# Kernel optimization log

Measured on AMD Instinct MI355X. Metric: run time of the kernel, lower is better.

## Reference

```python
import jax, jax.numpy as jnp
import numpy as np

H = 128  # LSTM units per direction


def _lstm_last_state(x_proj, Wr, b):
    """x_proj: [T,B,4H] precomputed input projection. Returns final hidden [B,H]."""
    B = x_proj.shape[1]
    h0 = jnp.zeros((B, H), x_proj.dtype)
    c0 = jnp.zeros((B, H), x_proj.dtype)

    def step(carry, xt):
        h, c = carry
        z = xt + h @ Wr + b  # [B,4H]
        i, f, g, o = jnp.split(z, 4, axis=-1)  # keras gate order: i, f, c(g), o
        i = jax.nn.sigmoid(i)
        f = jax.nn.sigmoid(f)
        g = jnp.tanh(g)
        o = jax.nn.sigmoid(o)
        c = f * c + i * g
        h = o * jnp.tanh(c)
        return (h, c), None

    (h, c), _ = jax.lax.scan(step, (h0, c0), x_proj)
    return h


def setup_inputs() -> dict:
    key = jax.random.key(0)
    ks = jax.random.split(key, 8)
    B, T, D = 128, 256, 1024
    s_in = 1.0 / np.sqrt(D)
    s_rec = 1.0 / np.sqrt(H)
    return {
        "x": jax.random.normal(ks[0], (B, T, D), jnp.float32),  # precomputed ELMo embeddings
        "Wf_k": jax.random.normal(ks[1], (D, 4 * H), jnp.float32) * s_in,
        "Wf_r": jax.random.normal(ks[2], (H, 4 * H), jnp.float32) * s_rec,
        "bf": jnp.zeros((4 * H,), jnp.float32),
        "Wb_k": jax.random.normal(ks[3], (D, 4 * H), jnp.float32) * s_in,
        "Wb_r": jax.random.normal(ks[4], (H, 4 * H), jnp.float32) * s_rec,
        "bb": jnp.zeros((4 * H,), jnp.float32),
        "W1": jax.random.normal(ks[5], (2 * H, 32), jnp.float32) * (1.0 / np.sqrt(2 * H)),
        "b1": jnp.zeros((32,), jnp.float32),
        "W2": jax.random.normal(ks[6], (32, 2), jnp.float32) * (1.0 / np.sqrt(32)),
        "b2": jnp.zeros((2,), jnp.float32),
    }


def reference(x, Wf_k, Wf_r, bf, Wb_k, Wb_r, bb, W1, b1, W2, b2):
    # Bidirectional LSTM over ELMo embeddings x: [B,T,D]; dropout inactive (inference).
    xp_f = jnp.einsum('btd,dg->tbg', x, Wf_k)            # [T,B,4H]
    h_fwd = _lstm_last_state(xp_f, Wf_r, bf)             # [B,H]
    xp_b = jnp.einsum('btd,dg->tbg', x[:, ::-1, :], Wb_k)
    h_bwd = _lstm_last_state(xp_b, Wb_r, bb)             # [B,H]
    h = jnp.concatenate([h_fwd, h_bwd], axis=-1)         # [B,2H]
    y = jax.nn.relu(h @ W1 + b1)                          # [B,32]
    return jax.nn.sigmoid(y @ W2 + b2)                    # [B,2]
```

## Files before the change

### kernel.cpp

```cpp
#include <hip/hip_runtime.h>
#include <cstdint>
#include <cstddef>


typedef __attribute__((ext_vector_type(8))) short short8;
typedef __attribute__((ext_vector_type(4))) float f32x4;
typedef __attribute__((address_space(1))) unsigned int gas_uint;
typedef __attribute__((address_space(3))) unsigned int las_uint;
typedef __attribute__((address_space(1))) const unsigned short as1_us;

__device__ __forceinline__ unsigned short f2b(float f) {
    unsigned int u = __float_as_uint(f);
    u += 0x7FFFu + ((u >> 16) & 1u);
    return (unsigned short)(u >> 16);
}
__device__ __forceinline__ float b2f(unsigned short u) {
    return __uint_as_float(((unsigned int)u) << 16);
}
__device__ __forceinline__ float rcp_(float x) { return __builtin_amdgcn_rcpf(x); }
__device__ __forceinline__ float sigmoidf_(float z) { return rcp_(1.0f + __expf(-z)); }
__device__ __forceinline__ float tanhf_(float z) {
    float e = __expf(2.0f * z);
    return 1.0f - 2.0f * rcp_(e + 1.0f);
}

#define LITE_BARRIER() asm volatile("s_waitcnt lgkmcnt(0)\n\ts_barrier" ::: "memory")

__device__ __forceinline__ void async_ld16(const unsigned short* g, unsigned short* l) {
    __builtin_amdgcn_global_load_lds(
        (gas_uint*)(uintptr_t)g,
        (las_uint*)(uintptr_t)(unsigned int)(uintptr_t)l,
        16, 0, 0);
}

__global__ void conv_x(const float* __restrict__ x, unsigned short* __restrict__ xb, int n8) {
    int idx = blockIdx.x * blockDim.x + threadIdx.x;
    int stride = gridDim.x * blockDim.x;
    for (int i = idx; i < n8; i += stride) {
        const float4* p = ((const float4*)x) + (size_t)i * 2;
        float4 a = p[0], b = p[1];
        short8 r;
        r[0] = (short)f2b(a.x); r[1] = (short)f2b(a.y);
        r[2] = (short)f2b(a.z); r[3] = (short)f2b(a.w);
        r[4] = (short)f2b(b.x); r[5] = (short)f2b(b.y);
        r[6] = (short)f2b(b.z); r[7] = (short)f2b(b.w);
        *(((short8*)xb) + i) = r;
    }
}

__global__ void conv_wk(const float* __restrict__ wf, const float* __restrict__ wb,
                        unsigned short* __restrict__ wt) {
    int dir = blockIdx.y;
    const float* w = dir ? wb : wf;
    int id = blockIdx.x * blockDim.x + threadIdx.x;
    int g = id >> 10, d = id & 1023;
    wt[(size_t)dir * 524288 + id] = f2b(w[d * 512 + g]);
}

__global__ __launch_bounds__(256, 2) void gemm_xp(
    const unsigned short* __restrict__ A,
    const unsigned short* __restrict__ Wt,
    const float* __restrict__ bf_, const float* __restrict__ bb_,
    unsigned short* __restrict__ XP)
{
    __shared__ unsigned short As[128 * 64];
    __shared__ unsigned short Bs[128 * 64];

    const int tid  = threadIdx.x;

    const int flat = blockIdx.x + 256 * (blockIdx.y + 4 * blockIdx.z);
    const int xcd  = flat & 7;
    const int p    = flat >> 3;
    const int tn   = p & 3;
    const int dir  = (p >> 2) & 1;
    const int tm   = xcd * 32 + (p >> 3);

    const int w    = tid >> 6;
    const int lane = tid & 63;
    const int lanelo = lane & 15;
    const int quad = lane >> 4;
    const int wm = w & 1, wn = w >> 1;

    const unsigned short* Bmat = Wt + (size_t)dir * 524288;
    const float* bias = dir ? bb_ : bf_;
    unsigned short* out = XP + (size_t)dir * 16777216;

    const unsigned short* ga[4];
    const unsigned short* gb[4];
    unsigned short* la[4];
    unsigned short* lb[4];
#pragma unroll
    for (int c = 0; c < 4; ++c) {
        int p2 = c * 256 + tid;
        int row = p2 >> 3;
        int lc = (p2 & 7) ^ (row & 7);
        ga[c] = A    + (size_t)(tm * 128 + row) * 1024 + lc * 8;
        gb[c] = Bmat + (size_t)(tn * 128 + row) * 1024 + lc * 8;
        int ub = (c * 256 + (tid & ~63)) * 8;
        la[c] = As + ub;
        lb[c] = Bs + ub;
    }

    f32x4 acc[4][4];
#pragma unroll
    for (int i = 0; i < 4; i++)
#pragma unroll
        for (int j = 0; j < 4; j++) acc[i][j] = (f32x4){0.f, 0.f, 0.f, 0.f};

    for (int kt = 0; kt < 16; ++kt) {
        __syncthreads();
#pragma unroll
        for (int c = 0; c < 4; ++c) {
            async_ld16(ga[c] + kt * 64, la[c]);
            async_ld16(gb[c] + kt * 64, lb[c]);
        }
        __syncthreads();
#pragma unroll
        for (int ks = 0; ks < 2; ++ks) {
            short8 af[4], bfr[4];
#pragma unroll
            for (int i = 0; i < 4; ++i) {
                int row = wm * 64 + i * 16 + lanelo;
                af[i] = *(const short8*)(As + row * 64 + (((ks * 4 + quad) ^ (row & 7)) * 8));
            }
#pragma unroll
            for (int j = 0; j < 4; ++j) {
                int row = wn * 64 + j * 16 + lanelo;
                bfr[j] = *(const short8*)(Bs + row * 64 + (((ks * 4 + quad) ^ (row & 7)) * 8));
            }
#pragma unroll
            for (int i = 0; i < 4; ++i)
#pragma unroll
                for (int j = 0; j < 4; ++j)
                    acc[i][j] = __builtin_amdgcn_mfma_f32_16x16x32_bf16(af[i], bfr[j], acc[i][j], 0, 0, 0);
        }
    }

    float biasv[4];
#pragma unroll
    for (int j = 0; j < 4; ++j)
        biasv[j] = bias[tn * 128 + wn * 64 + j * 16 + lanelo];

#pragma unroll
    for (int i = 0; i < 4; ++i) {
#pragma unroll
        for (int r = 0; r < 4; ++r) {
            int gr = tm * 128 + wm * 64 + i * 16 + quad * 4 + r;
            int bb = gr >> 8, tt = gr & 255;
            size_t orow = (size_t)(tt * 128 + bb) * 512;
#pragma unroll
            for (int j = 0; j < 4; ++j) {
                int col = tn * 128 + wn * 64 + j * 16 + lanelo;
                out[orow + col] = f2b(acc[i][j][r] + biasv[j]);
            }
        }
    }
}

__global__ __launch_bounds__(512, 2) void lstm_rec(
    const unsigned short* __restrict__ XP,
    const float* __restrict__ Wfr, const float* __restrict__ Wbr,
    float* __restrict__ Hout)
{
    __shared__ unsigned short h_lds[2][128];

    const int tid    = threadIdx.x;
    const int w      = tid >> 6;
    const int lane   = tid & 63;
    const int lanelo = lane & 15;
    const int quad   = lane >> 4;
    const int dir    = blockIdx.x >> 7;
    const int seq    = blockIdx.x & 127;
    const int dim    = w * 16 + lanelo;

    const float* Wr = dir ? Wbr : Wfr;
    const unsigned short* xp = XP + (size_t)dir * 16777216;

    short8 wrf[4][4];
#pragma unroll
    for (int g = 0; g < 4; ++g)
#pragma unroll
        for (int ks = 0; ks < 4; ++ks) {
            short8 f;
#pragma unroll
            for (int j = 0; j < 8; ++j)
                f[j] = (short)f2b(Wr[(size_t)(ks * 32 + quad * 8 + j) * 512 + g * 128 + dim]);
            wrf[g][ks] = f;
        }

    if (tid < 128) ((unsigned short*)h_lds)[tid] = 0;

    float cv = 0.f, hv = 0.f;

    const ptrdiff_t xstep = dir ? -65536 : 65536;
    const unsigned short* xb_ =
        xp + (size_t)(dir ? 255 : 0) * 65536 + (size_t)seq * 512 + dim;

    unsigned int xA[4], xB[4], xC[4], xD[4];

#define XLOAD(BUF)                                                               \
    {                                                                            \
        const as1_us* xg = (const as1_us*)(uintptr_t)xb_;                        \
        _Pragma("unroll")                                                        \
        for (int g = 0; g < 4; ++g) BUF[g] = xg[g * 128];                        \
        xb_ += xstep;                                                            \
    }

    XLOAD(xA)
    XLOAD(xB)
    XLOAD(xC)
    XLOAD(xD)

    LITE_BARRIER();

    const f32x4 kZ = (f32x4){0.f, 0.f, 0.f, 0.f};

#define LSTM_STEP(XC_, CUR, NXT)                                                 \
    {                                                                            \
               \
        float xv0 = b2f((unsigned short)XC_[0]);                                 \
        float xv1 = b2f((unsigned short)XC_[1]);                                 \
        float xv2 = b2f((unsigned short)XC_[2]);                                 \
        float xv3 = b2f((unsigned short)XC_[3]);                                 \
        XLOAD(XC_)                                                               \
         \
        short8 hfrag[4];                                                         \
        _Pragma("unroll")                                                        \
        for (int ks = 0; ks < 4; ++ks)                                           \
            hfrag[ks] = *(const short8*)(&h_lds[CUR][ks * 32 + quad * 8]);       \
            \
        f32x4 z0 = __builtin_amdgcn_mfma_f32_16x16x32_bf16(hfrag[0], wrf[0][0], kZ, 0, 0, 0); \
        f32x4 z1 = __builtin_amdgcn_mfma_f32_16x16x32_bf16(hfrag[0], wrf[1][0], kZ, 0, 0, 0); \
        f32x4 z2 = __builtin_amdgcn_mfma_f32_16x16x32_bf16(hfrag[0], wrf[2][0], kZ, 0, 0, 0); \
        f32x4 z3 = __builtin_amdgcn_mfma_f32_16x16x32_bf16(hfrag[0], wrf[3][0], kZ, 0, 0, 0); \
        _Pragma("unroll")                                                        \
        for (int ks = 1; ks < 4; ++ks) {                                         \
            z0 = __builtin_amdgcn_mfma_f32_16x16x32_bf16(hfrag[ks], wrf[0][ks], z0, 0, 0, 0); \
            z1 = __builtin_amdgcn_mfma_f32_16x16x32_bf16(hfrag[ks], wrf[1][ks], z1, 0, 0, 0); \
            z2 = __builtin_amdgcn_mfma_f32_16x16x32_bf16(hfrag[ks], wrf[2][ks], z2, 0, 0, 0); \
            z3 = __builtin_amdgcn_mfma_f32_16x16x32_bf16(hfrag[ks], wrf[3][ks], z3, 0, 0, 0); \
        }                                                                        \
                      \
        if (quad == 0) {                                                         \
            float zi = z0[0] + xv0, zf = z1[0] + xv1;                            \
            float zg = z2[0] + xv2, zo = z3[0] + xv3;                            \
            float iv = sigmoidf_(zi), fv = sigmoidf_(zf);                        \
            float gv = tanhf_(zg),    ov = sigmoidf_(zo);                        \
            cv = fv * cv + iv * gv;                                              \
            hv = ov * tanhf_(cv);                                                \
            h_lds[NXT][dim] = f2b(hv);                                           \
        }                                                                        \
        LITE_BARRIER();                                                          \
    }

    for (int t = 0; t < 256; t += 4) {
        LSTM_STEP(xA, 0, 1)
        LSTM_STEP(xB, 1, 0)
        LSTM_STEP(xC, 0, 1)
        LSTM_STEP(xD, 1, 0)
    }
#undef LSTM_STEP
#undef XLOAD

    if (quad == 0)
        Hout[(size_t)(dir * 128 + seq) * 128 + dim] = hv;
}

__global__ void mlp_head(const float* __restrict__ Hout,
                         const float* __restrict__ W1, const float* __restrict__ b1,
                         const float* __restrict__ W2, const float* __restrict__ b2,
                         float* __restrict__ out)
{
    __shared__ float y1[32];
    int b = blockIdx.x;
    int j = threadIdx.x;
    const float* hf = Hout + (size_t)b * 128;
    const float* hb = Hout + (size_t)(128 + b) * 128;
    if (j < 32) {
        float acc = b1[j];
        for (int k = 0; k < 128; ++k) acc += hf[k] * W1[k * 32 + j];
        for (int k = 0; k < 128; ++k) acc += hb[k] * W1[(128 + k) * 32 + j];
        y1[j] = fmaxf(acc, 0.0f);
    }
    __syncthreads();
    if (j < 2) {
        float z = b2[j];
        for (int k = 0; k < 32; ++k) z += y1[k] * W2[k * 2 + j];
        out[b * 2 + j] = 1.0f / (1.0f + __expf(-z));
    }
}

extern "C" void kernel_launch(void* const* d_in, const int* in_sizes, int n_in,
                              void* d_out, int out_size, void* d_ws, size_t ws_size,
                              hipStream_t stream) {
    const float* x    = (const float*)d_in[0];
    const float* Wf_k = (const float*)d_in[1];
    const float* Wf_r = (const float*)d_in[2];
    const float* bf   = (const float*)d_in[3];
    const float* Wb_k = (const float*)d_in[4];
    const float* Wb_r = (const float*)d_in[5];
    const float* bb   = (const float*)d_in[6];
    const float* W1   = (const float*)d_in[7];
    const float* b1   = (const float*)d_in[8];
    const float* W2   = (const float*)d_in[9];
    const float* b2   = (const float*)d_in[10];
    float* out = (float*)d_out;

    char* ws = (char*)d_ws;
    const size_t OFF_XB   = 0;
    const size_t OFF_WT   = 67108864;
    const size_t OFF_HOUT = OFF_WT + 2097152;
    const size_t OFF_XP   = OFF_HOUT + 131072;

    unsigned short* xb  = (unsigned short*)(ws + OFF_XB);
    unsigned short* wt  = (unsigned short*)(ws + OFF_WT);
    float*          ho  = (float*)(ws + OFF_HOUT);
    unsigned short* xpb = (unsigned short*)(ws + OFF_XP);

    conv_x<<<dim3(2048), dim3(256), 0, stream>>>(x, xb, 33554432 / 8);
    conv_wk<<<dim3(2048, 2), dim3(256), 0, stream>>>(Wf_k, Wb_k, wt);
    gemm_xp<<<dim3(256, 4, 2), dim3(256), 0, stream>>>(xb, wt, bf, bb, xpb);
    lstm_rec<<<dim3(256), dim3(512), 0, stream>>>(xpb, Wf_r, Wb_r, ho);
    mlp_head<<<dim3(128), dim3(64), 0, stream>>>(ho, W1, b1, W2, b2, out);
}
```

Measured before the change: 421.5 us.

## Fuse fp32-to-bf16 conversion of x into GEMM loader and register-prefetch A tiles

Removes the separate conv_x kernel and its 64MB bf16 scratch buffer. The GEMM now reads fp32 x straight into registers, prefetching the next K tile while the current one is used. It converts to bf16 and writes to LDS itself, using lighter barriers and explicit vmcnt waits. The LSTM step also loads h fragments only in lanes with lanelo==0 and keeps zero fragments elsewhere, cutting LDS reads. The GEMM reads twice the bytes per A tile, and 8 blocks (one per tn and dir) re-read each fp32 row tile instead of the cheaper bf16 copy.

```diff
diff --git a/kernel.cpp b/kernel.cpp
--- a/kernel.cpp
+++ b/kernel.cpp
@@ -31,21 +31,6 @@
         (gas_uint*)(uintptr_t)g,
         (las_uint*)(uintptr_t)(unsigned int)(uintptr_t)l,
         16, 0, 0);
-}
-
-__global__ void conv_x(const float* __restrict__ x, unsigned short* __restrict__ xb, int n8) {
-    int idx = blockIdx.x * blockDim.x + threadIdx.x;
-    int stride = gridDim.x * blockDim.x;
-    for (int i = idx; i < n8; i += stride) {
-        const float4* p = ((const float4*)x) + (size_t)i * 2;
-        float4 a = p[0], b = p[1];
-        short8 r;
-        r[0] = (short)f2b(a.x); r[1] = (short)f2b(a.y);
-        r[2] = (short)f2b(a.z); r[3] = (short)f2b(a.w);
-        r[4] = (short)f2b(b.x); r[5] = (short)f2b(b.y);
-        r[6] = (short)f2b(b.z); r[7] = (short)f2b(b.w);
-        *(((short8*)xb) + i) = r;
-    }
 }
 
 __global__ void conv_wk(const float* __restrict__ wf, const float* __restrict__ wb,
@@ -58,7 +43,7 @@
 }
 
 __global__ __launch_bounds__(256, 2) void gemm_xp(
-    const unsigned short* __restrict__ A,
+    const float* __restrict__ X,
     const unsigned short* __restrict__ Wt,
     const float* __restrict__ bf_, const float* __restrict__ bb_,
     unsigned short* __restrict__ XP)
@@ -85,7 +70,7 @@
     const float* bias = dir ? bb_ : bf_;
     unsigned short* out = XP + (size_t)dir * 16777216;
 
-    const unsigned short* ga[4];
+    const float* gax[4];
     const unsigned short* gb[4];
     unsigned short* la[4];
     unsigned short* lb[4];
@@ -94,11 +79,18 @@
         int p2 = c * 256 + tid;
         int row = p2 >> 3;
         int lc = (p2 & 7) ^ (row & 7);
-        ga[c] = A    + (size_t)(tm * 128 + row) * 1024 + lc * 8;
-        gb[c] = Bmat + (size_t)(tn * 128 + row) * 1024 + lc * 8;
+        gax[c] = X    + (size_t)(tm * 128 + row) * 1024 + lc * 8;
+        gb[c]  = Bmat + (size_t)(tn * 128 + row) * 1024 + lc * 8;
+        la[c]  = As + (size_t)p2 * 8;
         int ub = (c * 256 + (tid & ~63)) * 8;
-        la[c] = As + ub;
-        lb[c] = Bs + ub;
+        lb[c]  = Bs + ub;
+    }
+
+    float4 xr[4][2];
+#pragma unroll
+    for (int c = 0; c < 4; ++c) {
+        xr[c][0] = *(const float4*)(gax[c]);
+        xr[c][1] = *(const float4*)(gax[c] + 4);
     }
 
     f32x4 acc[4][4];
@@ -108,13 +100,32 @@
         for (int j = 0; j < 4; j++) acc[i][j] = (f32x4){0.f, 0.f, 0.f, 0.f};
 
     for (int kt = 0; kt < 16; ++kt) {
-        __syncthreads();
+        LITE_BARRIER();
 #pragma unroll
         for (int c = 0; c < 4; ++c) {
-            async_ld16(ga[c] + kt * 64, la[c]);
-            async_ld16(gb[c] + kt * 64, lb[c]);
-        }
-        __syncthreads();
+            short8 s;
+            s[0] = (short)f2b(xr[c][0].x); s[1] = (short)f2b(xr[c][0].y);
+            s[2] = (short)f2b(xr[c][0].z); s[3] = (short)f2b(xr[c][0].w);
+            s[4] = (short)f2b(xr[c][1].x); s[5] = (short)f2b(xr[c][1].y);
+            s[6] = (short)f2b(xr[c][1].z); s[7] = (short)f2b(xr[c][1].w);
+            *(short8*)la[c] = s;
+        }
+#pragma unroll
+        for (int c = 0; c < 4; ++c) async_ld16(gb[c] + kt * 64, lb[c]);
+        __builtin_amdgcn_sched_barrier(0);
+        if (kt < 15) {
+#pragma unroll
+            for (int c = 0; c < 4; ++c) {
+                xr[c][0] = *(const float4*)(gax[c] + (kt + 1) * 64);
+                xr[c][1] = *(const float4*)(gax[c] + (kt + 1) * 64 + 4);
+            }
+            __builtin_amdgcn_sched_barrier(0);
+            asm volatile("s_waitcnt vmcnt(8)" ::: "memory");
+        } else {
+            asm volatile("s_waitcnt vmcnt(0)" ::: "memory");
+        }
+        LITE_BARRIER();
+
 #pragma unroll
         for (int ks = 0; ks < 2; ++ks) {
             short8 af[4], bfr[4];
@@ -190,6 +201,11 @@
 
     if (tid < 128) ((unsigned short*)h_lds)[tid] = 0;
 
+    short8 hfrag[4];
+    const short8 hz = (short8){0, 0, 0, 0, 0, 0, 0, 0};
+#pragma unroll
+    for (int ks = 0; ks < 4; ++ks) hfrag[ks] = hz;
+
     float cv = 0.f, hv = 0.f;
 
     const ptrdiff_t xstep = dir ? -65536 : 65536;
@@ -223,12 +239,13 @@
         float xv2 = b2f((unsigned short)XC_[2]);                                 \
         float xv3 = b2f((unsigned short)XC_[3]);                                 \
         XLOAD(XC_)                                                               \
-         \
-        short8 hfrag[4];                                                         \
-        _Pragma("unroll")                                                        \
-        for (int ks = 0; ks < 4; ++ks)                                           \
-            hfrag[ks] = *(const short8*)(&h_lds[CUR][ks * 32 + quad * 8]);       \
-            \
+                                     \
+        if (lanelo == 0) {                                                       \
+            _Pragma("unroll")                                                    \
+            for (int ks = 0; ks < 4; ++ks)                                       \
+                hfrag[ks] = *(const short8*)(&h_lds[CUR][ks * 32 + quad * 8]);   \
+        }                                                                        \
+                               \
         f32x4 z0 = __builtin_amdgcn_mfma_f32_16x16x32_bf16(hfrag[0], wrf[0][0], kZ, 0, 0, 0); \
         f32x4 z1 = __builtin_amdgcn_mfma_f32_16x16x32_bf16(hfrag[0], wrf[1][0], kZ, 0, 0, 0); \
         f32x4 z2 = __builtin_amdgcn_mfma_f32_16x16x32_bf16(hfrag[0], wrf[2][0], kZ, 0, 0, 0); \
@@ -307,19 +324,16 @@
     float* out = (float*)d_out;
 
     char* ws = (char*)d_ws;
-    const size_t OFF_XB   = 0;
-    const size_t OFF_WT   = 67108864;
-    const size_t OFF_HOUT = OFF_WT + 2097152;
+    const size_t OFF_WT   = 0;
+    const size_t OFF_HOUT = 2097152;
     const size_t OFF_XP   = OFF_HOUT + 131072;
 
-    unsigned short* xb  = (unsigned short*)(ws + OFF_XB);
     unsigned short* wt  = (unsigned short*)(ws + OFF_WT);
     float*          ho  = (float*)(ws + OFF_HOUT);
     unsigned short* xpb = (unsigned short*)(ws + OFF_XP);
 
-    conv_x<<<dim3(2048), dim3(256), 0, stream>>>(x, xb, 33554432 / 8);
     conv_wk<<<dim3(2048, 2), dim3(256), 0, stream>>>(Wf_k, Wb_k, wt);
-    gemm_xp<<<dim3(256, 4, 2), dim3(256), 0, stream>>>(xb, wt, bf, bb, xpb);
+    gemm_xp<<<dim3(256, 4, 2), dim3(256), 0, stream>>>(x, wt, bf, bb, xpb);
     lstm_rec<<<dim3(256), dim3(512), 0, stream>>>(xpb, Wf_r, Wb_r, ho);
     mlp_head<<<dim3(128), dim3(64), 0, stream>>>(ho, W1, b1, W2, b2, out);
 }
```

Measured after the change: 419.0 us. Within noise of the previous version (-0.6%).
